# Optimization experiments

Measured on AMD Instinct MI355X. Metric: run time of the kernel, lower is better.

Reference implementation:

```python
import jax, jax.numpy as jnp
import numpy as np

B, L, E, H = 64, 2048, 300, 1  # batch, seq_len, embed_size, lstm hidden_size


def setup_inputs() -> dict:
    key = jax.random.key(0)
    ks = jax.random.split(key, 6)
    x = jax.random.normal(ks[0], (B, L, E), dtype=jnp.float32)
    source_lengths = jax.random.randint(ks[1], (B,), 0, L, dtype=jnp.int32)
    s = 1.0 / np.sqrt(H)  # pytorch LSTM init: U(-1/sqrt(H), 1/sqrt(H))
    W_ih = jax.random.uniform(ks[2], (4 * H, E), minval=-s, maxval=s, dtype=jnp.float32)
    W_hh = jax.random.uniform(ks[3], (4 * H, H), minval=-s, maxval=s, dtype=jnp.float32)
    b_ih = jax.random.uniform(ks[4], (4 * H,), minval=-s, maxval=s, dtype=jnp.float32)
    b_hh = jax.random.uniform(ks[5], (4 * H,), minval=-s, maxval=s, dtype=jnp.float32)
    return {"x": x, "source_lengths": source_lengths, "W_ih": W_ih, "W_hh": W_hh,
            "b_ih": b_ih, "b_hh": b_hh}


def _lstm_scores(x, W_ih, W_hh, b_ih, b_hh):
    # x: [B, L, E] -> hidden states [B, L, H]; pytorch gate order i, f, g, o.
    xg = jnp.einsum('ble,ge->blg', x, W_ih) + (b_ih + b_hh)  # [B, L, 4H]
    Bb = x.shape[0]
    Hh = W_hh.shape[1]
    h0 = jnp.zeros((Bb, Hh), x.dtype)
    c0 = jnp.zeros((Bb, Hh), x.dtype)

    def step(carry, g_t):
        h, c = carry
        gates = g_t + h @ W_hh.T  # [B, 4H]
        i, f, g, o = jnp.split(gates, 4, axis=-1)
        i = jax.nn.sigmoid(i)
        f = jax.nn.sigmoid(f)
        g = jnp.tanh(g)
        o = jax.nn.sigmoid(o)
        c = f * c + i * g
        h = o * jnp.tanh(c)
        return (h, c), h

    _, hs = jax.lax.scan(step, (h0, c0), jnp.swapaxes(xg, 0, 1))  # [L, B, H]
    return jnp.swapaxes(hs, 0, 1)  # [B, L, H]


def reference(x, source_lengths, W_ih, W_hh, b_ih, b_hh):
    hs = _lstm_scores(x, W_ih, W_hh, b_ih, b_hh)  # [B, L, 1]
    scores = hs[..., 0]  # squeeze -> [B, L]
    # Faithful to original (buggy) mask: only timestep 0 is masked to -inf,
    # and only when source_lengths[i] > 0.
    scores = scores.at[:, 0].set(jnp.where(source_lengths > 0, -jnp.inf, scores[:, 0]))
    attn = jax.nn.softmax(scores, axis=1)  # [B, L]
    # diag(attn) @ x == per-timestep broadcast scale
    return attn[:, :, None] * x  # [B, L, E]
```

## Files before the change

kernel.cpp:

```cpp
#include <hip/hip_runtime.h>
#include <math.h>

#define BATCH 64
#define SEQL  2048
#define EMB   300
#define NROWS (BATCH * SEQL)
#define NV4   (NROWS * 75)
#define U     8
#define CHUNK 16
#define WARM  48
#define NBLK  (SEQL / CHUNK)

typedef float floatx4 __attribute__((ext_vector_type(4)));

static __device__ __forceinline__ float fast_rcp(float x) {
#if __has_builtin(__builtin_amdgcn_rcpf)
    return __builtin_amdgcn_rcpf(x);
#else
    return 1.0f / x;
#endif
}

static __device__ __forceinline__ float fast_exp2(float x) {
#if __has_builtin(__builtin_amdgcn_exp2f)
    return __builtin_amdgcn_exp2f(x);
#else
    return exp2f(x);
#endif
}

__global__ void __launch_bounds__(256) proj_kernel(
    const float* __restrict__ x, const float* __restrict__ Wih,
    const float* __restrict__ bih, const float* __restrict__ bhh,
    float4* __restrict__ xg)
{
    const float L2E = 1.4426950408889634f;
    const int lane = threadIdx.x & 63;
    const int wid  = threadIdx.x >> 6;

    float4 w0[4], w1[4];
    float  bs[4];
#pragma unroll
    for (int k = 0; k < 4; ++k) {
        const float4* wr = (const float4*)(Wih + k * EMB);
        w0[k] = wr[lane];
        w1[k] = (lane < 11) ? wr[64 + lane] : make_float4(0.f, 0.f, 0.f, 0.f);
        bs[k] = bih[k] + bhh[k];
    }

    for (int row = blockIdx.x * 4 + wid; row < NROWS; row += gridDim.x * 4) {
        const float4* xr = (const float4*)(x + (size_t)row * EMB);
        float4 v0 = xr[lane];
        float4 v1 = (lane < 11) ? xr[64 + lane] : make_float4(0.f, 0.f, 0.f, 0.f);
        float acc[4];
#pragma unroll
        for (int k = 0; k < 4; ++k) {
            float a;
            a  = v0.x * w0[k].x; a = fmaf(v0.y, w0[k].y, a);
            a  = fmaf(v0.z, w0[k].z, a); a = fmaf(v0.w, w0[k].w, a);
            a  = fmaf(v1.x, w1[k].x, a); a = fmaf(v1.y, w1[k].y, a);
            a  = fmaf(v1.z, w1[k].z, a); a = fmaf(v1.w, w1[k].w, a);
            acc[k] = a;
        }
#pragma unroll
        for (int m = 32; m >= 1; m >>= 1) {
#pragma unroll
            for (int k = 0; k < 4; ++k) acc[k] += __shfl_xor(acc[k], m, 64);
        }
        if (lane == 0) {
            int t = row & (SEQL - 1);
            int bb = row >> 11;
            xg[t * BATCH + bb] = make_float4(
                -L2E * (acc[0] + bs[0]), -L2E * (acc[1] + bs[1]),
                -2.f * L2E * (acc[2] + bs[2]), -L2E * (acc[3] + bs[3]));
        }
    }
}

__global__ void __launch_bounds__(64) lstm_scan_kernel(
    const float4* __restrict__ xg, const int* __restrict__ slen,
    const float* __restrict__ Whh, float* __restrict__ score,
    float2* __restrict__ part)
{
    const float L2E = 1.4426950408889634f;
    const float K2  = -2.f * L2E;
    const int b = threadIdx.x;
    const int k = blockIdx.x;
    const float wi = -L2E * Whh[0];
    const float wf = -L2E * Whh[1];
    const float wg = K2   * Whh[2];
    const float wo = -L2E * Whh[3];
    const bool masked = slen[b] > 0;

    const int cstart = k * CHUNK;
    const int tstart = (cstart >= WARM) ? (cstart - WARM) : 0;
    const int nch    = (cstart + CHUNK - tstart) / U;

    float h = 0.f, c = 0.f;
    float m = -1e30f, sum = 0.f;

    float4 bufA[U], bufB[U];
#pragma unroll
    for (int u = 0; u < U; ++u) bufA[u] = xg[(tstart + u) * BATCH + b];

#define STEP(g4, T_) do {                                                  \
    float gi = fast_rcp(1.f + fast_exp2(fmaf(h, wi, (g4).x)));             \
    float gf = fast_rcp(1.f + fast_exp2(fmaf(h, wf, (g4).y)));             \
    float go = fast_rcp(1.f + fast_exp2(fmaf(h, wo, (g4).w)));             \
    float gg = fmaf(2.f, fast_rcp(1.f + fast_exp2(fmaf(h, wg, (g4).z))), -1.f); \
    float ig  = gi * gg;                                                   \
    float f2  = K2 * gf;                                                   \
    float ig2 = K2 * ig;                                                   \
    float targ = fmaf(f2, c, ig2);            \
    c = fmaf(gf, c, ig);                                                   \
    float tc = fmaf(2.f, fast_rcp(1.f + fast_exp2(targ)), -1.f);           \
    h = go * tc;                                                           \
    if (do_store) {                                                        \
        score[(T_) * BATCH + b] = h;                                       \
        if (!((T_) == 0 && masked)) {                                      \
            float mn = fmaxf(m, h);                                        \
            sum = fmaf(sum, fast_exp2((m - mn) * L2E),                     \
                       fast_exp2((h - mn) * L2E));                         \
            m = mn;                                                        \
        }                                                                  \
    }                                                                      \
} while (0)

    for (int ich = 0; ich < nch; ich += 2) {
        int tA = tstart + ich * U;
        int tB = tA + U;
#pragma unroll
        for (int u = 0; u < U; ++u)
            bufB[u] = xg[(tB + u) * BATCH + b];
        {
            const bool do_store = (tA >= cstart);
#pragma unroll
            for (int u = 0; u < U; ++u) STEP(bufA[u], tA + u);
        }
        if (ich + 2 < nch) {
#pragma unroll
            for (int u = 0; u < U; ++u)
                bufA[u] = xg[(tB + U + u) * BATCH + b];
        }
        {
            const bool do_store = (tB >= cstart);
#pragma unroll
            for (int u = 0; u < U; ++u) STEP(bufB[u], tB + u);
        }
    }
#undef STEP

    part[b * NBLK + k] = make_float2(m, sum);
}

__global__ void __launch_bounds__(64) reduce_kernel(
    const float2* __restrict__ part, float* __restrict__ stats)
{
    const float L2E = 1.4426950408889634f;
    const int b = blockIdx.x;
    const int l = threadIdx.x;

    float2 p0 = part[b * NBLK + l];
    float2 p1 = part[b * NBLK + 64 + l];

    float M = fmaxf(p0.x, p1.x);
    float sum = fmaf(p0.y, fast_exp2((p0.x - M) * L2E),
                     p1.y * fast_exp2((p1.x - M) * L2E));
#pragma unroll
    for (int sh = 32; sh >= 1; sh >>= 1) {
        float Mo = __shfl_xor(M, sh, 64);
        float so = __shfl_xor(sum, sh, 64);
        float Mn = fmaxf(M, Mo);
        sum = fmaf(sum, fast_exp2((M - Mn) * L2E),
                   so * fast_exp2((Mo - Mn) * L2E));
        M = Mn;
    }

    if (l == 0) {
        stats[b] = M;
        stats[BATCH + b] = fast_rcp(sum);
    }
}

__global__ void __launch_bounds__(256) scale_kernel(
    const float4* __restrict__ x4, const float* __restrict__ score,
    const float* __restrict__ stats, const int* __restrict__ slen,
    float4* __restrict__ out4)
{
    const float L2E = 1.4426950408889634f;
    const int stride = gridDim.x * blockDim.x;
    for (int idx = blockIdx.x * blockDim.x + threadIdx.x; idx < NV4; idx += stride) {
        unsigned row = (unsigned)idx / 75u;
        unsigned bb = row >> 11;
        unsigned t  = row & 2047u;
        float s = score[t * BATCH + bb];
        float a = fast_exp2((s - stats[bb]) * L2E) * stats[BATCH + bb];
        if (t == 0u && slen[bb] > 0) a = 0.f;
        float4 v = x4[idx];
        floatx4 r = {a * v.x, a * v.y, a * v.z, a * v.w};
        __builtin_nontemporal_store(r, (floatx4*)&out4[idx]);
    }
}

extern "C" void kernel_launch(void* const* d_in, const int* in_sizes, int n_in,
                              void* d_out, int out_size, void* d_ws, size_t ws_size,
                              hipStream_t stream)
{
    const float* x    = (const float*)d_in[0];
    const int*   slen = (const int*)d_in[1];
    const float* Wih  = (const float*)d_in[2];
    const float* Whh  = (const float*)d_in[3];
    const float* bih  = (const float*)d_in[4];
    const float* bhh  = (const float*)d_in[5];
    float* out = (float*)d_out;

    char* ws = (char*)d_ws;
    float4* xg    = (float4*)ws;
    float*  score = (float*)(ws + (size_t)NROWS * 16);
    float*  stats = (float*)(ws + (size_t)NROWS * 20);
    float2* part  = (float2*)(ws + (size_t)NROWS * 20 + 1024);

    proj_kernel<<<4096, 256, 0, stream>>>(x, Wih, bih, bhh, xg);
    lstm_scan_kernel<<<NBLK, 64, 0, stream>>>(xg, slen, Whh, score, part);
    reduce_kernel<<<BATCH, 64, 0, stream>>>(part, stats);
    scale_kernel<<<4096, 256, 0, stream>>>((const float4*)x, score, stats, slen,
                                           (float4*)out);
}
```

Measured before the change: 98.87 us.

## Compute input projection with one thread per row instead of wave-wide reduction

The projection kernel now gives each lane a whole (batch, timestep) row. Each thread loops over all 75 float4 chunks with four serial accumulators, which removes the cross-lane shuffle reduction and lets every lane write its own xg entry. The cost is that the x loads are no longer coalesced: adjacent lanes read rows 2048*300 floats apart, so each lane touches a separate cache line. Weight reads become uniform scalar or broadcast loads. The grid shrinks to 512 blocks.

Result: faster. 90.36 us (-8.6%).

```diff
diff --git a/kernel.cpp b/kernel.cpp
--- a/kernel.cpp
+++ b/kernel.cpp
@@ -36,45 +36,41 @@
 {
     const float L2E = 1.4426950408889634f;
     const int lane = threadIdx.x & 63;
-    const int wid  = threadIdx.x >> 6;
-
-    float4 w0[4], w1[4];
-    float  bs[4];
-#pragma unroll
-    for (int k = 0; k < 4; ++k) {
-        const float4* wr = (const float4*)(Wih + k * EMB);
-        w0[k] = wr[lane];
-        w1[k] = (lane < 11) ? wr[64 + lane] : make_float4(0.f, 0.f, 0.f, 0.f);
-        bs[k] = bih[k] + bhh[k];
-    }
-
-    for (int row = blockIdx.x * 4 + wid; row < NROWS; row += gridDim.x * 4) {
-        const float4* xr = (const float4*)(x + (size_t)row * EMB);
-        float4 v0 = xr[lane];
-        float4 v1 = (lane < 11) ? xr[64 + lane] : make_float4(0.f, 0.f, 0.f, 0.f);
-        float acc[4];
-#pragma unroll
-        for (int k = 0; k < 4; ++k) {
-            float a;
-            a  = v0.x * w0[k].x; a = fmaf(v0.y, w0[k].y, a);
-            a  = fmaf(v0.z, w0[k].z, a); a = fmaf(v0.w, w0[k].w, a);
-            a  = fmaf(v1.x, w1[k].x, a); a = fmaf(v1.y, w1[k].y, a);
-            a  = fmaf(v1.z, w1[k].z, a); a = fmaf(v1.w, w1[k].w, a);
-            acc[k] = a;
-        }
-#pragma unroll
-        for (int m = 32; m >= 1; m >>= 1) {
-#pragma unroll
-            for (int k = 0; k < 4; ++k) acc[k] += __shfl_xor(acc[k], m, 64);
-        }
-        if (lane == 0) {
-            int t = row & (SEQL - 1);
-            int bb = row >> 11;
-            xg[t * BATCH + bb] = make_float4(
-                -L2E * (acc[0] + bs[0]), -L2E * (acc[1] + bs[1]),
-                -2.f * L2E * (acc[2] + bs[2]), -L2E * (acc[3] + bs[3]));
-        }
-    }
+    const int t    = blockIdx.x * (blockDim.x >> 6) + (threadIdx.x >> 6);
+    if (t >= SEQL) return;
+
+    const float4* xr = (const float4*)(x + ((size_t)lane * SEQL + t) * EMB);
+
+    float acc0 = 0.f, acc1 = 0.f, acc2 = 0.f, acc3 = 0.f;
+#pragma unroll 3
+    for (int c = 0; c < 75; ++c) {
+        float4 v = xr[c];
+        const float* wc = Wih + 4 * c;
+        acc0 = fmaf(v.x, wc[0],           acc0);
+        acc0 = fmaf(v.y, wc[1],           acc0);
+        acc0 = fmaf(v.z, wc[2],           acc0);
+        acc0 = fmaf(v.w, wc[3],           acc0);
+        acc1 = fmaf(v.x, wc[EMB + 0],     acc1);
+        acc1 = fmaf(v.y, wc[EMB + 1],     acc1);
+        acc1 = fmaf(v.z, wc[EMB + 2],     acc1);
+        acc1 = fmaf(v.w, wc[EMB + 3],     acc1);
+        acc2 = fmaf(v.x, wc[2 * EMB + 0], acc2);
+        acc2 = fmaf(v.y, wc[2 * EMB + 1], acc2);
+        acc2 = fmaf(v.z, wc[2 * EMB + 2], acc2);
+        acc2 = fmaf(v.w, wc[2 * EMB + 3], acc2);
+        acc3 = fmaf(v.x, wc[3 * EMB + 0], acc3);
+        acc3 = fmaf(v.y, wc[3 * EMB + 1], acc3);
+        acc3 = fmaf(v.z, wc[3 * EMB + 2], acc3);
+        acc3 = fmaf(v.w, wc[3 * EMB + 3], acc3);
+    }
+
+    const float b0 = bih[0] + bhh[0];
+    const float b1 = bih[1] + bhh[1];
+    const float b2 = bih[2] + bhh[2];
+    const float b3 = bih[3] + bhh[3];
+    xg[t * BATCH + lane] = make_float4(
+        -L2E * (acc0 + b0), -L2E * (acc1 + b1),
+        -2.f * L2E * (acc2 + b2), -L2E * (acc3 + b3));
 }
 
 __global__ void __launch_bounds__(64) lstm_scan_kernel(
@@ -220,7 +216,7 @@
     float*  stats = (float*)(ws + (size_t)NROWS * 20);
     float2* part  = (float2*)(ws + (size_t)NROWS * 20 + 1024);
 
-    proj_kernel<<<4096, 256, 0, stream>>>(x, Wih, bih, bhh, xg);
+    proj_kernel<<<SEQL / 4, 256, 0, stream>>>(x, Wih, bih, bhh, xg);
     lstm_scan_kernel<<<NBLK, 64, 0, stream>>>(xg, slen, Whh, score, part);
     reduce_kernel<<<BATCH, 64, 0, stream>>>(part, stats);
     scale_kernel<<<4096, 256, 0, stream>>>((const float4*)x, score, stats, slen,
```
